# Kernel optimization log

Measured on AMD Instinct MI355X. Metric: run time of the kernel, lower is better.

## Reference

```python
import jax, jax.numpy as jnp
import numpy as np

# Complete 4-ary tree, leaves at depth 8, heap layout (children of i are 4i+1..4i+4).
B_ARY = 4
DEPTH = 8          # depths 0..8, leaves at depth 8
H = 512            # hidden_channels
IN = 512           # in_channels
OUT = 256          # out_channels
L = 2              # num_layers
LEVEL_STARTS = np.array([(B_ARY ** d - 1) // (B_ARY - 1) for d in range(DEPTH + 2)])
N = int(LEVEL_STARTS[-1])  # 87381


def setup_inputs() -> dict:
    key = jax.random.key(0)
    ks = jax.random.split(key, 12)
    x = jax.random.normal(ks[0], (N, IN), jnp.float32)

    # tree structure (numpy, deterministic)
    n_internal = int(LEVEL_STARTS[DEPTH])
    child_idx = np.zeros((N, B_ARY), np.int32)
    child_mask = np.zeros((N, B_ARY), np.int32)
    internal = np.arange(n_internal)
    child_idx[:n_internal] = (internal[:, None] * B_ARY + 1 + np.arange(B_ARY)[None, :]).astype(np.int32)
    child_mask[:n_internal] = 1
    node_parent = np.full(N, -1, np.int64)
    node_parent[1:] = (np.arange(1, N) - 1) // B_ARY
    node_depth = np.zeros(N, np.int64)
    for d in range(DEPTH + 1):
        node_depth[LEVEL_STARTS[d]:LEVEL_STARTS[d + 1]] = d
    is_leaf = node_depth == DEPTH
    edge_index = np.stack([np.arange(1, N), node_parent[1:]]).astype(np.int64)
    batch = np.zeros(N, np.int64)

    s = 0.02
    params = dict(
        W_in=jax.random.normal(ks[1], (IN, H), jnp.float32) * s,
        b_in=jnp.zeros((H,), jnp.float32),
        W_ioux=jax.random.normal(ks[2], (L, H, 3 * H), jnp.float32) * s,
        b_ioux=jnp.zeros((L, 3 * H), jnp.float32),
        W_iouh=jax.random.normal(ks[3], (L, H, 3 * H), jnp.float32) * s,
        b_iouh=jnp.zeros((L, 3 * H), jnp.float32),
        W_fx=jax.random.normal(ks[4], (L, H, H), jnp.float32) * s,
        b_fx=jnp.zeros((L, H), jnp.float32),
        W_fh=jax.random.normal(ks[5], (L, H, H), jnp.float32) * s,
        b_fh=jnp.zeros((L, H), jnp.float32),
        W_out=jax.random.normal(ks[6], (H, OUT), jnp.float32) * s,
        b_out=jnp.zeros((OUT,), jnp.float32),
    )
    return dict(
        x=x,
        edge_index=jnp.asarray(edge_index),
        batch=jnp.asarray(batch),
        node_depth=jnp.asarray(node_depth),
        node_parent=jnp.asarray(node_parent),
        is_leaf=jnp.asarray(is_leaf),
        child_idx=jnp.asarray(child_idx),
        child_mask=jnp.asarray(child_mask),
        **params,
    )


def reference(x, edge_index, batch, node_depth, node_parent, is_leaf,
              child_idx, child_mask,
              W_in, b_in, W_ioux, b_ioux, W_iouh, b_iouh,
              W_fx, b_fx, W_fh, b_fh, W_out, b_out):
    cm = child_mask.astype(x.dtype)  # [N, B]
    h = jax.nn.relu(x @ W_in + b_in)  # input projection (dropout = eval mode identity)
    for l in range(L):
        hidden = jnp.zeros((N, H), x.dtype)
        cell = jnp.zeros((N, H), x.dtype)
        # bottom-up over tree levels; levels are contiguous static slices
        for d in range(DEPTH, -1, -1):
            s, e = int(LEVEL_STARTS[d]), int(LEVEL_STARTS[d + 1])
            xl = h[s:e]                                   # [n_d, H]
            ci = child_idx[s:e]                           # [n_d, B]
            m = cm[s:e][..., None]                        # [n_d, B, 1]
            ch = hidden[ci] * m                           # masked child hidden
            cc = cell[ci] * m                             # masked child cell
            h_sum = ch.sum(axis=1)                        # child-sum
            iou = xl @ W_ioux[l] + b_ioux[l] + h_sum @ W_iouh[l] + b_iouh[l]
            i, o, u = jnp.split(iou, 3, axis=-1)
            i = jax.nn.sigmoid(i)
            o = jax.nn.sigmoid(o)
            u = jnp.tanh(u)
            f = jax.nn.sigmoid((xl @ W_fx[l] + b_fx[l])[:, None, :] + ch @ W_fh[l] + b_fh[l])
            c = i * u + (f * cc).sum(axis=1)
            hl = o * jnp.tanh(c)
            hidden = hidden.at[s:e].set(hl)
            cell = cell.at[s:e].set(c)
        h = hidden
    node_emb = h @ W_out + b_out                          # [N, OUT]
    tree_emb = jax.ops.segment_sum(node_emb, batch, num_segments=1)  # 'sum' aggregation
    return node_emb, tree_emb
```

## Files before the change

kernel.cpp:

```cpp
#include <hip/hip_runtime.h>

typedef __bf16 bf16;
typedef __bf16 bf16x8 __attribute__((ext_vector_type(8)));
typedef float f32x4 __attribute__((ext_vector_type(4)));

#define NN 87381
#define NINT 21845
#define NLEAF 65536
#define LEAF_START 21845

__device__ __forceinline__ float sigmoidf_(float x) {
    return 1.0f / (1.0f + __expf(-x));
}
__device__ __forceinline__ float tanhf_(float x) {
    return 1.0f - 2.0f / (__expf(2.0f * x) + 1.0f);
}

__device__ __forceinline__ void gload_lds16(const bf16* g, bf16* l) {
    __builtin_amdgcn_global_load_lds(
        (const __attribute__((address_space(1))) unsigned int*)g,
        (__attribute__((address_space(3))) unsigned int*)l, 16, 0, 0);
}

__device__ __forceinline__ int xcd_swz(int bid, int nwg) {
    int q = nwg >> 3, r = nwg & 7;
    int x = bid & 7, i = bid >> 3;
    return (x < r ? x * (q + 1) : r * (q + 1) + (x - r) * q) + i;
}

#define SWZ(r, kc) ((((r) << 3) | ((kc) ^ ((r) & 7))) << 3)

__global__ void tconv_kernel(const float* __restrict__ W, bf16* __restrict__ Wt,
                             int NR, int total) {
    int idx = blockIdx.x * 256 + threadIdx.x;
    if (idx >= total) return;
    int n = idx >> 9;
    int k = idx & 511;
    Wt[idx] = (bf16)W[(size_t)k * NR + n];
}

__global__ void convx_kernel(const float* __restrict__ X, bf16* __restrict__ Y, int total4) {
    int idx = blockIdx.x * 256 + threadIdx.x;
    if (idx >= total4) return;
    const float4 f = *reinterpret_cast<const float4*>(X + (size_t)idx * 4);
    bf16 o[4] = {(bf16)f.x, (bf16)f.y, (bf16)f.z, (bf16)f.w};
    *reinterpret_cast<ushort2*>(Y + (size_t)idx * 4 + 0) = *reinterpret_cast<ushort2*>(&o[0]);
    *reinterpret_cast<ushort2*>(Y + (size_t)idx * 4 + 2) = *reinterpret_cast<ushort2*>(&o[2]);
}

#define MFMA_COMPUTE_2x4(As, Bs, acc, wm, wn, lm, quad)                          \
    _Pragma("unroll")                                                            \
    for (int kk = 0; kk < 64; kk += 32) {                                        \
        const int kc_ = (kk >> 3) + quad;                                        \
        bf16x8 areg[2], breg[4];                                                 \
        _Pragma("unroll")                                                        \
        for (int mi = 0; mi < 2; ++mi)                                           \
            areg[mi] = *reinterpret_cast<const bf16x8*>(                         \
                &(As)[SWZ(wm + mi * 16 + lm, kc_)]);                             \
        _Pragma("unroll")                                                        \
        for (int ni = 0; ni < 4; ++ni)                                           \
            breg[ni] = *reinterpret_cast<const bf16x8*>(                         \
                &(Bs)[SWZ(wn + ni * 16 + lm, kc_)]);                             \
        _Pragma("unroll")                                                        \
        for (int mi = 0; mi < 2; ++mi)                                           \
            _Pragma("unroll")                                                    \
            for (int ni = 0; ni < 4; ++ni)                                       \
                acc[mi][ni] = __builtin_amdgcn_mfma_f32_16x16x32_bf16(           \
                    areg[mi], breg[ni], acc[mi][ni], 0, 0, 0);                   \
    }

__global__ __launch_bounds__(512)
void gemm_kernel(const bf16* __restrict__ A, const bf16* __restrict__ Bt,
                 int bstride, int K, int ntiles,
                 float* __restrict__ Cf, bf16* __restrict__ Cb,
                 const float* __restrict__ bias1, const float* __restrict__ bias2,
                 int M, int N, int relu, int swz)
{
    __shared__ __align__(16) bf16 As[2][128 * 64];
    __shared__ __align__(16) bf16 Bs[2][128 * 64];
    const int tid  = threadIdx.x;
    const int wave = tid >> 6;
    const int lane = tid & 63;
    int bid = blockIdx.x;
    if (swz) bid = xcd_swz(bid, (int)gridDim.x);
    const int bm = (bid / ntiles) * 128;
    const int bn = (bid % ntiles) * 128;
    const int wm = (wave & 3) * 32;
    const int wn = (wave >> 2) * 64;
    const int lm   = lane & 15;
    const int quad = lane >> 4;

    f32x4 acc[2][4];
#pragma unroll
    for (int i = 0; i < 2; ++i)
#pragma unroll
        for (int j = 0; j < 4; ++j) acc[i][j] = (f32x4){0.f, 0.f, 0.f, 0.f};

    const bf16* aptr[2];
    const bf16* bptr[2];
    int loff[2];
#pragma unroll
    for (int i = 0; i < 2; ++i) {
        int c   = i * 512 + tid;
        int r   = c >> 3;
        int kc8 = ((c & 7) ^ (r & 7)) << 3;
        int gr  = bm + r; gr = (gr < M) ? gr : (M - 1);
        aptr[i] = A + (size_t)gr * K + kc8;
        bptr[i] = Bt + (size_t)(bn + r) * bstride + kc8;
        loff[i] = c << 3;
    }

    auto stage = [&](int buf, int t) {
        const int kofs = t << 6;
#pragma unroll
        for (int i = 0; i < 2; ++i)
            gload_lds16(aptr[i] + kofs, &As[0][0] + buf * (128 * 64) + loff[i]);
#pragma unroll
        for (int i = 0; i < 2; ++i)
            gload_lds16(bptr[i] + kofs, &Bs[0][0] + buf * (128 * 64) + loff[i]);
    };

    const int nk = K >> 6;
    stage(0, 0);
    __syncthreads();
    int cur = 0;
    for (int t = 0; t < nk; ++t) {
        if (t + 1 < nk) stage(cur ^ 1, t + 1);
        MFMA_COMPUTE_2x4(As[cur], Bs[cur], acc, wm, wn, lm, quad);
        __syncthreads();
        cur ^= 1;
    }

#pragma unroll
    for (int ni = 0; ni < 4; ++ni) {
        int col = bn + wn + ni * 16 + lm;
        float bsum = (bias1 ? bias1[col] : 0.f) + (bias2 ? bias2[col] : 0.f);
#pragma unroll
        for (int mi = 0; mi < 2; ++mi) {
#pragma unroll
            for (int r = 0; r < 4; ++r) {
                int row = bm + wm + mi * 16 + quad * 4 + r;
                if (row < M) {
                    float v = acc[mi][ni][r] + bsum;
                    if (relu) v = (v > 0.f) ? v : 0.f;
                    if (Cf) Cf[(size_t)row * N + col] = v;
                    else    Cb[(size_t)row * N + col] = (bf16)v;
                }
            }
        }
    }
}

__global__ __launch_bounds__(512)
void leaf_kernel(const bf16* __restrict__ A, const bf16* __restrict__ wiou,
                 const float* __restrict__ bx1, const float* __restrict__ bx2,
                 bf16* __restrict__ hout, bf16* __restrict__ cellout,
                 bf16* __restrict__ hsout, int M, int swz)
{
    __shared__ __align__(16) bf16 As[2][128 * 64];
    __shared__ __align__(16) bf16 Bs[2][3 * 64 * 64];
    const int tid  = threadIdx.x;
    const int wave = tid >> 6;
    const int lane = tid & 63;
    int bid = blockIdx.x;
    if (swz) bid = xcd_swz(bid, (int)gridDim.x);
    const int bm = (bid >> 3) * 128;
    const int bn = (bid & 7) * 64;
    if (bm >= M) return;
    const int wm   = (wave & 3) * 32;
    const int wn   = (wave >> 2) * 32;
    const int lm   = lane & 15;
    const int quad = lane >> 4;

    f32x4 acc[3][2][2];
#pragma unroll
    for (int g = 0; g < 3; ++g)
#pragma unroll
        for (int i = 0; i < 2; ++i)
#pragma unroll
            for (int j = 0; j < 2; ++j) acc[g][i][j] = (f32x4){0.f, 0.f, 0.f, 0.f};

    const bf16* aptr[2];
    int aoff[2];
#pragma unroll
    for (int i = 0; i < 2; ++i) {
        int c   = i * 512 + tid;
        int r   = c >> 3;
        int kc8 = ((c & 7) ^ (r & 7)) << 3;
        int gr  = bm + r; gr = (gr < M) ? gr : (M - 1);
        aptr[i] = A + ((size_t)gr << 9) + kc8;
        aoff[i] = c << 3;
    }
    const bf16* bptr[3];
    int boff[3];
#pragma unroll
    for (int i = 0; i < 3; ++i) {
        int c   = i * 512 + tid;
        int g   = c >> 9;
        int cg  = c & 511;
        int r   = cg >> 3;
        int kc8 = ((cg & 7) ^ (r & 7)) << 3;
        bptr[i] = wiou + (size_t)(g * 512 + bn + r) * 512 + kc8;
        boff[i] = c << 3;
    }

    auto stage = [&](int buf, int t) {
        const int kofs = t << 6;
#pragma unroll
        for (int i = 0; i < 2; ++i)
            gload_lds16(aptr[i] + kofs, &As[0][0] + buf * (128 * 64) + aoff[i]);
#pragma unroll
        for (int i = 0; i < 3; ++i)
            gload_lds16(bptr[i] + kofs, &Bs[0][0] + buf * (3 * 64 * 64) + boff[i]);
    };

    stage(0, 0);
    __syncthreads();
    int cur = 0;
    for (int t = 0; t < 8; ++t) {
        if (t + 1 < 8) stage(cur ^ 1, t + 1);
#pragma unroll
        for (int kk = 0; kk < 64; kk += 32) {
            const int kc_ = (kk >> 3) + quad;
            bf16x8 areg[2];
#pragma unroll
            for (int mi = 0; mi < 2; ++mi)
                areg[mi] = *reinterpret_cast<const bf16x8*>(
                    &As[cur][SWZ(wm + mi * 16 + lm, kc_)]);
            bf16x8 breg[3][2];
#pragma unroll
            for (int g = 0; g < 3; ++g)
#pragma unroll
                for (int ni = 0; ni < 2; ++ni)
                    breg[g][ni] = *reinterpret_cast<const bf16x8*>(
                        &Bs[cur][g * 4096 + SWZ(wn + ni * 16 + lm, kc_)]);
#pragma unroll
            for (int g = 0; g < 3; ++g)
#pragma unroll
                for (int mi = 0; mi < 2; ++mi)
#pragma unroll
                    for (int ni = 0; ni < 2; ++ni)
                        acc[g][mi][ni] = __builtin_amdgcn_mfma_f32_16x16x32_bf16(
                            areg[mi], breg[g][ni], acc[g][mi][ni], 0, 0, 0);
        }
        __syncthreads();
        cur ^= 1;
    }

#pragma unroll
    for (int ni = 0; ni < 2; ++ni) {
        int col = bn + wn + ni * 16 + lm;
        float bi = bx1[col]        + bx2[col];
        float bo = bx1[col + 512]  + bx2[col + 512];
        float bu = bx1[col + 1024] + bx2[col + 1024];
#pragma unroll
        for (int mi = 0; mi < 2; ++mi) {
            int rbase = bm + wm + mi * 16 + quad * 4;
            float hsum = 0.f;
#pragma unroll
            for (int r = 0; r < 4; ++r) {
                int row = rbase + r;
                if (row < M) {
                    float i_ = sigmoidf_(acc[0][mi][ni][r] + bi);
                    float o_ = sigmoidf_(acc[1][mi][ni][r] + bo);
                    float u_ = tanhf_(acc[2][mi][ni][r] + bu);
                    float c  = i_ * u_;
                    bf16 hb  = (bf16)(o_ * tanhf_(c));
                    cellout[(size_t)row * 512 + col] = (bf16)c;
                    hout[(size_t)row * 512 + col] = hb;
                    hsum += (float)hb;
                }
            }
            if (hsout && rbase < M)
                hsout[(size_t)(rbase >> 2) * 512 + col] = (bf16)hsum;
        }
    }
}

__global__ __launch_bounds__(512)
void level_kernel(const bf16* __restrict__ hs, const bf16* __restrict__ hc,
                  const bf16* __restrict__ cellc,
                  const bf16* __restrict__ wih, const bf16* __restrict__ wfh,
                  const bf16* __restrict__ xout,
                  const float* __restrict__ bx1, const float* __restrict__ bx2,
                  const float* __restrict__ bf1, const float* __restrict__ bf2,
                  float* __restrict__ fcsum,
                  bf16* __restrict__ hout, bf16* __restrict__ cellout,
                  bf16* __restrict__ hsout, int E, int swz)
{
    __shared__ __align__(16) bf16 As[2][128 * 64];
    __shared__ __align__(16) bf16 Bs[2][3 * 64 * 64];
    const int tid  = threadIdx.x;
    const int wave = tid >> 6;
    const int lane = tid & 63;
    int bid = blockIdx.x;
    if (swz) bid = xcd_swz(bid, (int)gridDim.x);
    const int bm = (bid >> 3) * 128;
    const int bn = (bid & 7);
    if (bm >= E) return;
    const int lm   = lane & 15;
    const int quad = lane >> 4;
    const int M4   = 4 * E;

    {
        const int wmA = (wave & 3) * 32;
        const int wnA = (wave >> 2) * 32;
        const int rb  = tid >> 3;
        const int kcb = ((tid & 7) ^ (rb & 7)) << 3;
        const bf16* bfp = wfh + (size_t)(bn * 64 + rb) * 512 + kcb;
        const int  bofs = tid << 3;

        for (int s = 0; s < 4; ++s) {
            const bf16* aptrA[2]; int aoffA[2];
#pragma unroll
            for (int i = 0; i < 2; ++i) {
                int c   = i * 512 + tid;
                int r   = c >> 3;
                int kc8 = ((c & 7) ^ (r & 7)) << 3;
                int gr  = 4 * bm + 128 * s + r; gr = (gr < M4) ? gr : (M4 - 1);
                aptrA[i] = hc + ((size_t)gr << 9) + kc8;
                aoffA[i] = c << 3;
            }
            f32x4 accA[2][2];
#pragma unroll
            for (int i = 0; i < 2; ++i)
#pragma unroll
                for (int j = 0; j < 2; ++j) accA[i][j] = (f32x4){0.f, 0.f, 0.f, 0.f};

            auto stageA = [&](int buf, int t) {
                const int kofs = t << 6;
#pragma unroll
                for (int i = 0; i < 2; ++i)
                    gload_lds16(aptrA[i] + kofs, &As[0][0] + buf * (128 * 64) + aoffA[i]);
                gload_lds16(bfp + kofs, &Bs[0][0] + buf * (3 * 64 * 64) + bofs);
            };

            stageA(0, 0);
            __syncthreads();
            int cur = 0;
            for (int t = 0; t < 8; ++t) {
                if (t + 1 < 8) stageA(cur ^ 1, t + 1);
#pragma unroll
                for (int kk = 0; kk < 64; kk += 32) {
                    const int kc_ = (kk >> 3) + quad;
                    bf16x8 ar[2], br[2];
#pragma unroll
                    for (int mi = 0; mi < 2; ++mi)
                        ar[mi] = *reinterpret_cast<const bf16x8*>(
                            &As[cur][SWZ(wmA + mi * 16 + lm, kc_)]);
#pragma unroll
                    for (int ni = 0; ni < 2; ++ni)
                        br[ni] = *reinterpret_cast<const bf16x8*>(
                            &Bs[cur][SWZ(wnA + ni * 16 + lm, kc_)]);
#pragma unroll
                    for (int mi = 0; mi < 2; ++mi)
#pragma unroll
                        for (int ni = 0; ni < 2; ++ni)
                            accA[mi][ni] = __builtin_amdgcn_mfma_f32_16x16x32_bf16(
                                ar[mi], br[ni], accA[mi][ni], 0, 0, 0);
                }
                __syncthreads();
                cur ^= 1;
            }
#pragma unroll
            for (int ni = 0; ni < 2; ++ni) {
                int col = bn * 64 + wnA + ni * 16 + lm;
                float bsum = bf1[col] + bf2[col];
#pragma unroll
                for (int mi = 0; mi < 2; ++mi) {
                    int lr = 128 * s + wmA + mi * 16 + quad * 4;
                    int p  = bm + (lr >> 2);
                    if (p < E) {
                        float pf = (float)xout[(size_t)p * 2048 + 1536 + col] + bsum;
                        float fc = 0.f;
#pragma unroll
                        for (int r = 0; r < 4; ++r) {
                            int cr = 4 * bm + lr + r;
                            fc += sigmoidf_(accA[mi][ni][r] + pf) *
                                  (float)cellc[(size_t)cr * 512 + col];
                        }
                        fcsum[(size_t)p * 512 + col] = fc;
                    }
                }
            }
        }
    }

    const int wm = (wave & 3) * 32;
    const int wn = (wave >> 2) * 32;
    const int bncol = bn * 64;

    f32x4 acc[3][2][2];
#pragma unroll
    for (int g = 0; g < 3; ++g)
#pragma unroll
        for (int i = 0; i < 2; ++i)
#pragma unroll
            for (int j = 0; j < 2; ++j) acc[g][i][j] = (f32x4){0.f, 0.f, 0.f, 0.f};

    const bf16* aptr[2];
    int aoff[2];
#pragma unroll
    for (int i = 0; i < 2; ++i) {
        int c   = i * 512 + tid;
        int r   = c >> 3;
        int kc8 = ((c & 7) ^ (r & 7)) << 3;
        int gr  = bm + r; gr = (gr < E) ? gr : (E - 1);
        aptr[i] = hs + ((size_t)gr << 9) + kc8;
        aoff[i] = c << 3;
    }
    const bf16* bptr[3];
    int boff[3];
#pragma unroll
    for (int i = 0; i < 3; ++i) {
        int c   = i * 512 + tid;
        int g   = c >> 9;
        int cg  = c & 511;
        int r   = cg >> 3;
        int kc8 = ((cg & 7) ^ (r & 7)) << 3;
        bptr[i] = wih + (size_t)(g * 512 + bncol + r) * 512 + kc8;
        boff[i] = c << 3;
    }

    auto stage = [&](int buf, int t) {
        const int kofs = t << 6;
#pragma unroll
        for (int i = 0; i < 2; ++i)
            gload_lds16(aptr[i] + kofs, &As[0][0] + buf * (128 * 64) + aoff[i]);
#pragma unroll
        for (int i = 0; i < 3; ++i)
            gload_lds16(bptr[i] + kofs, &Bs[0][0] + buf * (3 * 64 * 64) + boff[i]);
    };

    stage(0, 0);
    __syncthreads();
    int cur = 0;
    for (int t = 0; t < 8; ++t) {
        if (t + 1 < 8) stage(cur ^ 1, t + 1);
#pragma unroll
        for (int kk = 0; kk < 64; kk += 32) {
            const int kc_ = (kk >> 3) + quad;
            bf16x8 areg[2];
#pragma unroll
            for (int mi = 0; mi < 2; ++mi)
                areg[mi] = *reinterpret_cast<const bf16x8*>(
                    &As[cur][SWZ(wm + mi * 16 + lm, kc_)]);
            bf16x8 breg[3][2];
#pragma unroll
            for (int g = 0; g < 3; ++g)
#pragma unroll
                for (int ni = 0; ni < 2; ++ni)
                    breg[g][ni] = *reinterpret_cast<const bf16x8*>(
                        &Bs[cur][g * 4096 + SWZ(wn + ni * 16 + lm, kc_)]);
#pragma unroll
            for (int g = 0; g < 3; ++g)
#pragma unroll
                for (int mi = 0; mi < 2; ++mi)
#pragma unroll
                    for (int ni = 0; ni < 2; ++ni)
                        acc[g][mi][ni] = __builtin_amdgcn_mfma_f32_16x16x32_bf16(
                            areg[mi], breg[g][ni], acc[g][mi][ni], 0, 0, 0);
        }
        __syncthreads();
        cur ^= 1;
    }

#pragma unroll
    for (int ni = 0; ni < 2; ++ni) {
        int col = bncol + wn + ni * 16 + lm;
        float bi = bx1[col]        + bx2[col];
        float bo = bx1[col + 512]  + bx2[col + 512];
        float bu = bx1[col + 1024] + bx2[col + 1024];
#pragma unroll
        for (int mi = 0; mi < 2; ++mi) {
            int rbase = bm + wm + mi * 16 + quad * 4;
            float hsum = 0.f;
#pragma unroll
            for (int r = 0; r < 4; ++r) {
                int row = rbase + r;
                if (row < E) {
                    float ax  = (float)xout[(size_t)row * 2048 + col];
                    float aox = (float)xout[(size_t)row * 2048 + 512 + col];
                    float aux = (float)xout[(size_t)row * 2048 + 1024 + col];
                    float i_ = sigmoidf_(acc[0][mi][ni][r] + ax + bi);
                    float o_ = sigmoidf_(acc[1][mi][ni][r] + aox + bo);
                    float u_ = tanhf_(acc[2][mi][ni][r] + aux + bu);
                    float c  = i_ * u_ + fcsum[(size_t)row * 512 + col];
                    bf16 hb  = (bf16)(o_ * tanhf_(c));
                    cellout[(size_t)row * 512 + col] = (bf16)c;
                    hout[(size_t)row * 512 + col] = hb;
                    hsum += (float)hb;
                }
            }
            if (hsout && rbase < E)
                hsout[(size_t)(rbase >> 2) * 512 + col] = (bf16)hsum;
        }
    }
}

#define R1_BLOCKS 2048
#define R1_ROWS 43
__global__ void reduce1_kernel(const float* __restrict__ ne, float* __restrict__ partial)
{
    int t = threadIdx.x;
    int b = blockIdx.x;
    int r0 = b * R1_ROWS;
    int r1 = r0 + R1_ROWS; r1 = (r1 < NN) ? r1 : NN;
    float acc = 0.f;
    for (int r = r0; r < r1; ++r) acc += ne[(size_t)r * 256 + t];
    partial[(size_t)b * 256 + t] = acc;
}
__global__ void reduce2_kernel(const float* __restrict__ partial, float* __restrict__ partial2)
{
    int t = threadIdx.x;
    int b = blockIdx.x;
    float acc = 0.f;
    for (int i = 0; i < 32; ++i) acc += partial[(size_t)(b * 32 + i) * 256 + t];
    partial2[(size_t)b * 256 + t] = acc;
}
__global__ void reduce3_kernel(const float* __restrict__ partial2, float* __restrict__ tree)
{
    int t = threadIdx.x;
    float acc = 0.f;
    for (int i = 0; i < 64; ++i) acc += partial2[(size_t)i * 256 + t];
    tree[t] = acc;
}

extern "C" void kernel_launch(void* const* d_in, const int* in_sizes, int n_in,
                              void* d_out, int out_size, void* d_ws, size_t ws_size,
                              hipStream_t stream)
{
    const float* x      = (const float*)d_in[0];
    const float* W_in   = (const float*)d_in[8];
    const float* b_in   = (const float*)d_in[9];
    const float* W_ioux = (const float*)d_in[10];
    const float* b_ioux = (const float*)d_in[11];
    const float* W_iouh = (const float*)d_in[12];
    const float* b_iouh = (const float*)d_in[13];
    const float* W_fx   = (const float*)d_in[14];
    const float* b_fx   = (const float*)d_in[15];
    const float* W_fh   = (const float*)d_in[16];
    const float* b_fh   = (const float*)d_in[17];
    const float* W_out  = (const float*)d_in[18];
    const float* b_out  = (const float*)d_in[19];

    static const int LS[10] = {0, 1, 5, 21, 85, 341, 1365, 5461, 21845, 87381};

    char* ws = (char*)d_ws;
    size_t off = 0;
    auto take = [&](size_t bytes) -> void* {
        void* p = ws + off;
        off += (bytes + 255) & ~(size_t)255;
        return p;
    };
    bf16*  wt_in      = (bf16*) take((size_t)512 * 512 * 2);
    bf16*  wt_out     = (bf16*) take((size_t)256 * 512 * 2);
    bf16*  wt_xcat    = (bf16*) take((size_t)2 * 2048 * 512 * 2);
    bf16*  wt_iouh    = (bf16*) take((size_t)2 * 1536 * 512 * 2);
    bf16*  wt_fh      = (bf16*) take((size_t)2 * 512 * 512 * 2);
    bf16*  h          = (bf16*) take((size_t)NN * 512 * 2);
    bf16*  hint1      = (bf16*) take((size_t)NINT * 512 * 2);
    bf16*  hB         = (bf16*) take((size_t)NLEAF * 512 * 2);
    bf16*  cell_int   = (bf16*) take((size_t)NINT * 512 * 2);
    bf16*  cell_leaf  = (bf16*) take((size_t)NLEAF * 512 * 2);
    float* fcsum      = (float*)take((size_t)16384 * 512 * 4);
    bf16*  hsA        = (bf16*) take((size_t)16384 * 512 * 2);
    bf16*  hsB        = (bf16*) take((size_t)4096 * 512 * 2);
    bf16*  XOUT       = (bf16*) take((size_t)NINT * 2048 * 2);
    float* partial    = (float*)take((size_t)R1_BLOCKS * 256 * 4);
    float* partial2   = (float*)take((size_t)64 * 256 * 4);
    bf16*  xbf        = cell_int;

    dim3 blk(256), blk512(512);
    auto tgrid = [](int total) { return dim3((unsigned)((total + 255) / 256)); };

    tconv_kernel<<<tgrid(512 * 512), blk, 0, stream>>>(W_in, wt_in, 512, 512 * 512);
    tconv_kernel<<<tgrid(256 * 512), blk, 0, stream>>>(W_out, wt_out, 256, 256 * 512);
    for (int l = 0; l < 2; ++l) {
        bf16* xc = wt_xcat + (size_t)l * 2048 * 512;
        tconv_kernel<<<tgrid(1536 * 512), blk, 0, stream>>>(
            W_ioux + (size_t)l * 512 * 1536, xc, 1536, 1536 * 512);
        tconv_kernel<<<tgrid(512 * 512), blk, 0, stream>>>(
            W_fx + (size_t)l * 512 * 512, xc + (size_t)1536 * 512, 512, 512 * 512);
        tconv_kernel<<<tgrid(1536 * 512), blk, 0, stream>>>(
            W_iouh + (size_t)l * 512 * 1536, wt_iouh + (size_t)l * 1536 * 512,
            1536, 1536 * 512);
        tconv_kernel<<<tgrid(512 * 512), blk, 0, stream>>>(
            W_fh + (size_t)l * 512 * 512, wt_fh + (size_t)l * 512 * 512,
            512, 512 * 512);
    }

    auto gemm = [&](const bf16* A, const bf16* Bt, int bstride, int K,
                    float* Cf, bf16* Cb, const float* b1, const float* b2,
                    int M, int N, int relu, int swz) {
        int mt = (M + 127) / 128, nt = N / 128;
        gemm_kernel<<<dim3((unsigned)(mt * nt)), blk512, 0, stream>>>(
            A, Bt, bstride, K, nt, Cf, Cb, b1, b2, M, N, relu, swz);
    };

    convx_kernel<<<tgrid(NN * 128), blk, 0, stream>>>(x, xbf, NN * 128);
    gemm(xbf, wt_in, 512, 512, nullptr, h, b_in, nullptr, NN, 512, 1, 1);

    for (int l = 0; l < 2; ++l) {
        const bf16* wxc  = wt_xcat + (size_t)l * 2048 * 512;
        const bf16* wih  = wt_iouh + (size_t)l * 1536 * 512;
        const bf16* wfh  = wt_fh + (size_t)l * 512 * 512;
        const float* bx1 = b_ioux + (size_t)l * 1536;
        const float* bx2 = b_iouh + (size_t)l * 1536;
        const float* bf1 = b_fx + (size_t)l * 512;
        const float* bf2 = b_fh + (size_t)l * 512;

        const bf16* lin   = (l == 0) ? (h + (size_t)LEAF_START * 512) : hB;
        bf16*       lout  = (l == 0) ? hB : (h + (size_t)LEAF_START * 512);
        const bf16* hprev = (l == 0) ? h : hint1;
        bf16*       hcur  = (l == 0) ? hint1 : h;

        gemm(hprev, wxc, 512, 512, nullptr, XOUT, nullptr, nullptr,
             NINT, 2048, 0, 1);

        {
            int mt = NLEAF / 128;
            leaf_kernel<<<dim3((unsigned)(mt * 8)), blk512, 0, stream>>>(
                lin, wxc , bx1, bx2,
                lout, cell_leaf, hsA, NLEAF, 1);
        }

        for (int d = 7; d >= 0; --d) {
            int s  = LS[d];
            int E  = LS[d + 1] - LS[d];
            int cs = LS[d + 1];
            const bf16* hc = (d == 7) ? lout : (hcur + (size_t)cs * 512);
            const bf16* cc = (d == 7) ? cell_leaf : (cell_int + (size_t)cs * 512);
            bf16* hs_read  = (d & 1) ? hsA : hsB;
            bf16* hs_write = (d == 0) ? nullptr : ((d & 1) ? hsB : hsA);
            const bf16* xo = XOUT + (size_t)s * 2048;

            int mt = (E + 127) / 128;
            level_kernel<<<dim3((unsigned)(mt * 8)), blk512, 0, stream>>>(
                hs_read, hc, cc, wih, wfh, xo, bx1, bx2, bf1, bf2, fcsum,
                hcur + (size_t)s * 512, cell_int + (size_t)s * 512, hs_write, E, 1);
        }
    }

    float* node_emb = (float*)d_out;
    gemm(h, wt_out, 512, 512, node_emb, nullptr, b_out, nullptr, NN, 256, 0, 1);
    reduce1_kernel<<<dim3(R1_BLOCKS), blk, 0, stream>>>(node_emb, partial);
    reduce2_kernel<<<dim3(64), blk, 0, stream>>>(partial, partial2);
    reduce3_kernel<<<dim3(1), blk, 0, stream>>>(partial2, node_emb + (size_t)NN * 256);
}
```

Baseline: 1.831 ms.

## Split fused level kernel into separate forget-gate and IOU GEMM kernels

```diff
diff --git a/kernel.cpp b/kernel.cpp
--- a/kernel.cpp
+++ b/kernel.cpp
@@ -278,15 +278,12 @@
 }
 
 __global__ __launch_bounds__(512)
-void level_kernel(const bf16* __restrict__ hs, const bf16* __restrict__ hc,
-                  const bf16* __restrict__ cellc,
-                  const bf16* __restrict__ wih, const bf16* __restrict__ wfh,
-                  const bf16* __restrict__ xout,
-                  const float* __restrict__ bx1, const float* __restrict__ bx2,
-                  const float* __restrict__ bf1, const float* __restrict__ bf2,
-                  float* __restrict__ fcsum,
-                  bf16* __restrict__ hout, bf16* __restrict__ cellout,
-                  bf16* __restrict__ hsout, int E, int swz)
+void iou_fused_kernel(const bf16* __restrict__ A, const bf16* __restrict__ wiou,
+                      const float* __restrict__ bx1, const float* __restrict__ bx2,
+                      const float* __restrict__ fcs, const bf16* __restrict__ xout,
+                      bf16* __restrict__ hout, bf16* __restrict__ cellout,
+                      bf16* __restrict__ hsout,
+                      int M, int swz)
 {
     __shared__ __align__(16) bf16 As[2][128 * 64];
     __shared__ __align__(16) bf16 Bs[2][3 * 64 * 64];
@@ -296,99 +293,12 @@
     int bid = blockIdx.x;
     if (swz) bid = xcd_swz(bid, (int)gridDim.x);
     const int bm = (bid >> 3) * 128;
-    const int bn = (bid & 7);
-    if (bm >= E) return;
+    const int bn = (bid & 7) * 64;
+    if (bm >= M) return;
+    const int wm   = (wave & 3) * 32;
+    const int wn   = (wave >> 2) * 32;
     const int lm   = lane & 15;
     const int quad = lane >> 4;
-    const int M4   = 4 * E;
-
-    {
-        const int wmA = (wave & 3) * 32;
-        const int wnA = (wave >> 2) * 32;
-        const int rb  = tid >> 3;
-        const int kcb = ((tid & 7) ^ (rb & 7)) << 3;
-        const bf16* bfp = wfh + (size_t)(bn * 64 + rb) * 512 + kcb;
-        const int  bofs = tid << 3;
-
-        for (int s = 0; s < 4; ++s) {
-            const bf16* aptrA[2]; int aoffA[2];
-#pragma unroll
-            for (int i = 0; i < 2; ++i) {
-                int c   = i * 512 + tid;
-                int r   = c >> 3;
-                int kc8 = ((c & 7) ^ (r & 7)) << 3;
-                int gr  = 4 * bm + 128 * s + r; gr = (gr < M4) ? gr : (M4 - 1);
-                aptrA[i] = hc + ((size_t)gr << 9) + kc8;
-                aoffA[i] = c << 3;
-            }
-            f32x4 accA[2][2];
-#pragma unroll
-            for (int i = 0; i < 2; ++i)
-#pragma unroll
-                for (int j = 0; j < 2; ++j) accA[i][j] = (f32x4){0.f, 0.f, 0.f, 0.f};
-
-            auto stageA = [&](int buf, int t) {
-                const int kofs = t << 6;
-#pragma unroll
-                for (int i = 0; i < 2; ++i)
-                    gload_lds16(aptrA[i] + kofs, &As[0][0] + buf * (128 * 64) + aoffA[i]);
-                gload_lds16(bfp + kofs, &Bs[0][0] + buf * (3 * 64 * 64) + bofs);
-            };
-
-            stageA(0, 0);
-            __syncthreads();
-            int cur = 0;
-            for (int t = 0; t < 8; ++t) {
-                if (t + 1 < 8) stageA(cur ^ 1, t + 1);
-#pragma unroll
-                for (int kk = 0; kk < 64; kk += 32) {
-                    const int kc_ = (kk >> 3) + quad;
-                    bf16x8 ar[2], br[2];
-#pragma unroll
-                    for (int mi = 0; mi < 2; ++mi)
-                        ar[mi] = *reinterpret_cast<const bf16x8*>(
-                            &As[cur][SWZ(wmA + mi * 16 + lm, kc_)]);
-#pragma unroll
-                    for (int ni = 0; ni < 2; ++ni)
-                        br[ni] = *reinterpret_cast<const bf16x8*>(
-                            &Bs[cur][SWZ(wnA + ni * 16 + lm, kc_)]);
-#pragma unroll
-                    for (int mi = 0; mi < 2; ++mi)
-#pragma unroll
-                        for (int ni = 0; ni < 2; ++ni)
-                            accA[mi][ni] = __builtin_amdgcn_mfma_f32_16x16x32_bf16(
-                                ar[mi], br[ni], accA[mi][ni], 0, 0, 0);
-                }
-                __syncthreads();
-                cur ^= 1;
-            }
-#pragma unroll
-            for (int ni = 0; ni < 2; ++ni) {
-                int col = bn * 64 + wnA + ni * 16 + lm;
-                float bsum = bf1[col] + bf2[col];
-#pragma unroll
-                for (int mi = 0; mi < 2; ++mi) {
-                    int lr = 128 * s + wmA + mi * 16 + quad * 4;
-                    int p  = bm + (lr >> 2);
-                    if (p < E) {
-                        float pf = (float)xout[(size_t)p * 2048 + 1536 + col] + bsum;
-                        float fc = 0.f;
-#pragma unroll
-                        for (int r = 0; r < 4; ++r) {
-                            int cr = 4 * bm + lr + r;
-                            fc += sigmoidf_(accA[mi][ni][r] + pf) *
-                                  (float)cellc[(size_t)cr * 512 + col];
-                        }
-                        fcsum[(size_t)p * 512 + col] = fc;
-                    }
-                }
-            }
-        }
-    }
-
-    const int wm = (wave & 3) * 32;
-    const int wn = (wave >> 2) * 32;
-    const int bncol = bn * 64;
 
     f32x4 acc[3][2][2];
 #pragma unroll
@@ -405,8 +315,8 @@
         int c   = i * 512 + tid;
         int r   = c >> 3;
         int kc8 = ((c & 7) ^ (r & 7)) << 3;
-        int gr  = bm + r; gr = (gr < E) ? gr : (E - 1);
-        aptr[i] = hs + ((size_t)gr << 9) + kc8;
+        int gr  = bm + r; gr = (gr < M) ? gr : (M - 1);
+        aptr[i] = A + ((size_t)gr << 9) + kc8;
         aoff[i] = c << 3;
     }
     const bf16* bptr[3];
@@ -418,7 +328,7 @@
         int cg  = c & 511;
         int r   = cg >> 3;
         int kc8 = ((cg & 7) ^ (r & 7)) << 3;
-        bptr[i] = wih + (size_t)(g * 512 + bncol + r) * 512 + kc8;
+        bptr[i] = wiou + (size_t)(g * 512 + bn + r) * 512 + kc8;
         boff[i] = c << 3;
     }
 
@@ -467,7 +377,7 @@
 
 #pragma unroll
     for (int ni = 0; ni < 2; ++ni) {
-        int col = bncol + wn + ni * 16 + lm;
+        int col = bn + wn + ni * 16 + lm;
         float bi = bx1[col]        + bx2[col];
         float bo = bx1[col + 512]  + bx2[col + 512];
         float bu = bx1[col + 1024] + bx2[col + 1024];
@@ -478,22 +388,107 @@
 #pragma unroll
             for (int r = 0; r < 4; ++r) {
                 int row = rbase + r;
-                if (row < E) {
+                if (row < M) {
                     float ax  = (float)xout[(size_t)row * 2048 + col];
                     float aox = (float)xout[(size_t)row * 2048 + 512 + col];
                     float aux = (float)xout[(size_t)row * 2048 + 1024 + col];
                     float i_ = sigmoidf_(acc[0][mi][ni][r] + ax + bi);
                     float o_ = sigmoidf_(acc[1][mi][ni][r] + aox + bo);
                     float u_ = tanhf_(acc[2][mi][ni][r] + aux + bu);
-                    float c  = i_ * u_ + fcsum[(size_t)row * 512 + col];
+                    float c  = i_ * u_ + fcs[(size_t)row * 512 + col];
                     bf16 hb  = (bf16)(o_ * tanhf_(c));
                     cellout[(size_t)row * 512 + col] = (bf16)c;
                     hout[(size_t)row * 512 + col] = hb;
                     hsum += (float)hb;
                 }
             }
-            if (hsout && rbase < E)
+            if (hsout && rbase < M)
                 hsout[(size_t)(rbase >> 2) * 512 + col] = (bf16)hsum;
+        }
+    }
+}
+
+__global__ __launch_bounds__(512)
+void cf_kernel(const bf16* __restrict__ hc, const bf16* __restrict__ cellc,
+               const bf16* __restrict__ wfh, const bf16* __restrict__ xout,
+               const float* __restrict__ bf1, const float* __restrict__ bf2,
+               float* __restrict__ fcs, int E, int swz)
+{
+    const int M = 4 * E;
+    __shared__ __align__(16) bf16 As[2][128 * 64];
+    __shared__ __align__(16) bf16 Bs[2][128 * 64];
+    const int tid  = threadIdx.x;
+    const int wave = tid >> 6;
+    const int lane = tid & 63;
+    int bid = blockIdx.x;
+    if (swz) bid = xcd_swz(bid, (int)gridDim.x);
+    const int bm = (bid >> 2) * 128;
+    const int bn = (bid & 3) * 128;
+    if (bm >= M) return;
+    const int wm   = (wave & 3) * 32;
+    const int wn   = (wave >> 2) * 64;
+    const int lm   = lane & 15;
+    const int quad = lane >> 4;
+
+    f32x4 acc[2][4];
+#pragma unroll
+    for (int i = 0; i < 2; ++i)
+#pragma unroll
+        for (int j = 0; j < 4; ++j) acc[i][j] = (f32x4){0.f, 0.f, 0.f, 0.f};
+
+    const bf16* aptr[2];
+    const bf16* bptr[2];
+    int loff[2];
+#pragma unroll
+    for (int i = 0; i < 2; ++i) {
+        int c   = i * 512 + tid;
+        int r   = c >> 3;
+        int kc8 = ((c & 7) ^ (r & 7)) << 3;
+        int gr  = bm + r; gr = (gr < M) ? gr : (M - 1);
+        aptr[i] = hc + ((size_t)gr << 9) + kc8;
+        bptr[i] = wfh + (size_t)(bn + r) * 512 + kc8;
+        loff[i] = c << 3;
+    }
+
+    auto stage = [&](int buf, int t) {
+        const int kofs = t << 6;
+#pragma unroll
+        for (int i = 0; i < 2; ++i)
+            gload_lds16(aptr[i] + kofs, &As[0][0] + buf * (128 * 64) + loff[i]);
+#pragma unroll
+        for (int i = 0; i < 2; ++i)
+            gload_lds16(bptr[i] + kofs, &Bs[0][0] + buf * (128 * 64) + loff[i]);
+    };
+
+    stage(0, 0);
+    __syncthreads();
+    int cur = 0;
+    for (int t = 0; t < 8; ++t) {
+        if (t + 1 < 8) stage(cur ^ 1, t + 1);
+        MFMA_COMPUTE_2x4(As[cur], Bs[cur], acc, wm, wn, lm, quad);
+        __syncthreads();
+        cur ^= 1;
+    }
+
+#pragma unroll
+    for (int ni = 0; ni < 4; ++ni) {
+        int col = bn + wn + ni * 16 + lm;
+        float bsum = bf1[col] + bf2[col];
+#pragma unroll
+        for (int mi = 0; mi < 2; ++mi) {
+            int R0 = bm + wm + mi * 16;
+            if (R0 + quad * 4 < M) {
+                int p = (R0 >> 2) + quad;
+                float pf = (float)xout[(size_t)p * 2048 + 1536 + col] + bsum;
+                float fc = 0.f;
+#pragma unroll
+                for (int r = 0; r < 4; ++r) {
+                    int row = R0 + quad * 4 + r;
+                    fc += sigmoidf_(acc[mi][ni][r] + pf) *
+                          (float)cellc[(size_t)row * 512 + col];
+                }
+                fcs[(size_t)p * 512 + col] = fc;
+            }
         }
     }
 }
@@ -635,9 +630,13 @@
             bf16* hs_write = (d == 0) ? nullptr : ((d & 1) ? hsB : hsA);
             const bf16* xo = XOUT + (size_t)s * 2048;
 
-            int mt = (E + 127) / 128;
-            level_kernel<<<dim3((unsigned)(mt * 8)), blk512, 0, stream>>>(
-                hs_read, hc, cc, wih, wfh, xo, bx1, bx2, bf1, bf2, fcsum,
+            int mt_cf = (4 * E + 127) / 128;
+            cf_kernel<<<dim3((unsigned)(mt_cf * 4)), blk512, 0, stream>>>(
+                hc, cc, wfh, xo, bf1, bf2, fcsum, E, 1);
+
+            int mt_iou = (E + 127) / 128;
+            iou_fused_kernel<<<dim3((unsigned)(mt_iou * 8)), blk512, 0, stream>>>(
+                hs_read, wih, bx1, bx2, fcsum, xo,
                 hcur + (size_t)s * 512, cell_int + (size_t)s * 512, hs_write, E, 1);
         }
     }
```

New measurement: 1.673 ms. 8.6% less time.
